# Kernel tuning notes

Hardware: AMD Instinct MI355X
Metric: run time of the kernel (lower is better)

## Reference

```python
import jax, jax.numpy as jnp
import numpy as np

NUM_HEADS = 8
DIM = 192  # target_dim = min(channels_list)
CHANNELS = [192, 384, 768]
SIZES = [(32, 32), (16, 16), (8, 8)]
BATCH = 4


def conv1x1(x, w, b):
    # x: [B,C,H,W], w: [O,C,1,1], b: [O]
    y = jnp.einsum('bchw,oc->bohw', x, w[:, :, 0, 0])
    return y + b[None, :, None, None]


def cross_attention(x, ctx, wq, wkv, wp, bp):
    # x: [B,N,C] queries, ctx: [B,M,C] key/value source
    B, N, C = x.shape
    M = ctx.shape[1]
    h = NUM_HEADS
    d = C // h
    scale = d ** -0.5
    q = (x @ wq.T).reshape(B, N, h, d).transpose(0, 2, 1, 3)          # [B,h,N,d]
    kv = ctx @ wkv.T                                                   # [B,M,2C]
    k = kv[..., :C].reshape(B, M, h, d).transpose(0, 2, 1, 3)          # [B,h,M,d]
    v = kv[..., C:].reshape(B, M, h, d).transpose(0, 2, 1, 3)          # [B,h,M,d]
    attn = jax.nn.softmax(jnp.einsum('bhnd,bhmd->bhnm', q, k) * scale, axis=-1)
    o = jnp.einsum('bhnm,bhmd->bhnd', attn, v)
    o = o.transpose(0, 2, 1, 3).reshape(B, N, C)
    return o @ wp.T + bp


def setup_inputs() -> dict:
    key = jax.random.key(0)
    ks = iter(jax.random.split(key, 64))
    s = 0.02
    inp = {}
    for i, (c, (H, W)) in enumerate(zip(CHANNELS, SIZES)):
        inp[f'f{i}'] = jax.random.normal(next(ks), (BATCH, c, H, W), dtype=jnp.float32)
    # input projections (scale 0 has c == target_dim -> Identity, no params)
    for i in (1, 2):
        c = CHANNELS[i]
        inp[f'proj{i}_w'] = jax.random.normal(next(ks), (DIM, c, 1, 1), dtype=jnp.float32) * s
        inp[f'proj{i}_b'] = jnp.zeros((DIM,), dtype=jnp.float32)
    # cross-attention params per scale (qkv_bias=False; proj has bias)
    for i in range(3):
        inp[f'q{i}_w'] = jax.random.normal(next(ks), (DIM, DIM), dtype=jnp.float32) * s
        inp[f'kv{i}_w'] = jax.random.normal(next(ks), (2 * DIM, DIM), dtype=jnp.float32) * s
        inp[f'pr{i}_w'] = jax.random.normal(next(ks), (DIM, DIM), dtype=jnp.float32) * s
        inp[f'pr{i}_b'] = jnp.zeros((DIM,), dtype=jnp.float32)
    # output projections back to each channel count
    for i, c in enumerate(CHANNELS):
        inp[f'out{i}_w'] = jax.random.normal(next(ks), (c, DIM, 1, 1), dtype=jnp.float32) * s
        inp[f'out{i}_b'] = jnp.zeros((c,), dtype=jnp.float32)
    return inp


def _forward(f0, f1, f2,
             proj1_w, proj1_b, proj2_w, proj2_b,
             q0_w, kv0_w, pr0_w, pr0_b,
             q1_w, kv1_w, pr1_w, pr1_b,
             q2_w, kv2_w, pr2_w, pr2_b,
             out0_w, out0_b, out1_w, out1_b, out2_w, out2_b):
    projected = [
        f0,  # Identity (channels == target_dim)
        conv1x1(f1, proj1_w, proj1_b),
        conv1x1(f2, proj2_w, proj2_b),
    ]
    attn_params = [
        (q0_w, kv0_w, pr0_w, pr0_b),
        (q1_w, kv1_w, pr1_w, pr1_b),
        (q2_w, kv2_w, pr2_w, pr2_b),
    ]
    out_params = [(out0_w, out0_b), (out1_w, out1_b), (out2_w, out2_b)]
    outputs = []
    for i in range(3):
        feat = projected[i]
        B, C, H, W = feat.shape
        x = feat.reshape(B, C, H * W).transpose(0, 2, 1)  # [B,N,C]
        ctxs = []
        for j in range(3):
            if j != i:
                r = jax.image.resize(projected[j], (B, C, H, W), method='bilinear', antialias=False)
                ctxs.append(r.reshape(B, C, H * W).transpose(0, 2, 1))
        ctx = jnp.concatenate(ctxs, axis=1)  # [B,M,C]
        enh = cross_attention(x, ctx, *attn_params[i])
        enh = enh.transpose(0, 2, 1).reshape(B, C, H, W) + feat
        outputs.append(conv1x1(enh, *out_params[i]))
    return tuple(outputs)


def reference(f0, f1, f2,
              proj1_w, proj1_b, proj2_w, proj2_b,
              q0_w, kv0_w, pr0_w, pr0_b,
              q1_w, kv1_w, pr1_w, pr1_b,
              q2_w, kv2_w, pr2_w, pr2_b,
              out0_w, out0_b, out1_w, out1_b, out2_w, out2_b):
    return _forward(f0, f1, f2,
                    proj1_w, proj1_b, proj2_w, proj2_b,
                    q0_w, kv0_w, pr0_w, pr0_b,
                    q1_w, kv1_w, pr1_w, pr1_b,
                    q2_w, kv2_w, pr2_w, pr2_b,
                    out0_w, out0_b, out1_w, out1_b, out2_w, out2_b)
```

## Files before the change

kernel.cpp:

```cpp
#include <hip/hip_runtime.h>
#include <math.h>

#define BB 4
#define DIM 192
#define HEADS 8
#define HD 24

typedef __attribute__((ext_vector_type(8))) short short8v;
typedef __attribute__((ext_vector_type(4))) short short4v;
typedef __attribute__((ext_vector_type(4))) float f32x4;
typedef __attribute__((ext_vector_type(4))) unsigned uint4v;

__device__ __forceinline__ short f2bf(float f) {
  unsigned u = __builtin_bit_cast(unsigned, f);
  u += 0x7FFF + ((u >> 16) & 1);
  return (short)(u >> 16);
}
__device__ __forceinline__ unsigned pk2(float a, float b) {
  unsigned r;
  asm("v_cvt_pk_bf16_f32 %0, %1, %2" : "=v"(r) : "v"(a), "v"(b));
  return r;
}
__device__ __forceinline__ float bf2f(unsigned u16) {
  return __builtin_bit_cast(float, u16 << 16);
}
__device__ __forceinline__ void gl_lds16(const void* g, void* l) {
  __builtin_amdgcn_global_load_lds(
      (const __attribute__((address_space(1))) unsigned int*)g,
      (__attribute__((address_space(3))) unsigned int*)l, 16, 0, 0);
}
__device__ __forceinline__ int xcd_swz(int bid, int nwg) {
  int q = nwg >> 3, r = nwg & 7;
  int xcd = bid & 7, idx = bid >> 3;
  return (xcd < r) ? (xcd * (q + 1) + idx) : (r * (q + 1) + (xcd - r) * q + idx);
}

struct PJob {
  int type;
  const float* s0; const float* s1; const float* s2;
  void* dst;
  int P0, P1v;
  int t_begin, t_end;
};
struct PJobs { PJob j[20]; };

__global__ __launch_bounds__(256) void prep_k(PJobs jobs, int nj) {
  int tid = blockIdx.x * 256 + threadIdx.x;
  for (int ji = 0; ji < 20; ++ji) {
    if (ji >= nj) return;
    PJob g = jobs.j[ji];
    if (tid < g.t_begin || tid >= g.t_end) continue;
    int t = tid - g.t_begin;
    if (g.type == 0) {
      float4 v = *(const float4*)&g.s0[(size_t)t * 4];
      uint2 u = {pk2(v.x, v.y), pk2(v.z, v.w)};
      *(uint2*)&((short*)g.dst)[(size_t)t * 4] = u;
    } else if (g.type == 1) {
      int X = g.P0, C = g.P1v, C8 = C >> 3;
      int x = t % X, c8 = (t / X) % C8, b = t / (X * C8);
      const float* s = g.s0 + ((size_t)b * C + c8 * 8) * X + x;
      float v[8];
#pragma unroll
      for (int j = 0; j < 8; ++j) v[j] = s[(size_t)j * X];
      uint4 u = {pk2(v[0], v[1]), pk2(v[2], v[3]), pk2(v[4], v[5]), pk2(v[6], v[7])};
      *(uint4*)&((short*)g.dst)[((size_t)b * X + x) * C + c8 * 8] = u;
    } else {
      int o = t;
      const float* w = g.s0 + (size_t)o * 192;
      float acc = g.s2[o];
      for (int k = 0; k < 192; ++k) acc += w[k] * g.s1[k];
      ((float*)g.dst)[o] = acc;
    }
    return;
  }
}

struct MJob {
  const short* A; const short* W; const float* bias; const float* T;
  void* out;
  int K, nOT, mode, tokPerB;
  float scale;
  int blk_begin, blk_end;
};
struct MJobs { MJob j[10]; };

__global__ __launch_bounds__(256) void mgemm_k(MJobs jobs, int nj, int nwg) {
  __shared__ short Asl[64 * 192];
  __shared__ short Wsl[64 * 192];
  int blk = xcd_swz(blockIdx.x, nwg);
  for (int ji = 0; ji < 10; ++ji) {
    if (ji >= nj) return;
    MJob g = jobs.j[ji];
    if (blk < g.blk_begin || blk >= g.blk_end) continue;
    int lb = blk - g.blk_begin;
    int ot = lb % g.nOT, tt = lb / g.nOT;
    int t0 = tt * 64, o0 = ot * 64;
    int tid = threadIdx.x, wv = tid >> 6, lane = tid & 63, c = lane & 15, qi = lane >> 4;
    const int K = g.K;
    int rowK[6];
#pragma unroll
    for (int i = 0; i < 6; ++i) {
      int o16 = i * 256 + tid;
      int row = o16 / 24, ch = o16 - row * 24;
      rowK[i] = row * K + ((ch ^ (row & 7)) << 3);
    }
    const short* Ab = g.A + (size_t)t0 * K;
    const short* Wb = g.W + (size_t)o0 * K;
    f32x4 acc[4];
#pragma unroll
    for (int jj = 0; jj < 4; ++jj) acc[jj] = (f32x4){0.f, 0.f, 0.f, 0.f};
    int nkc = K / 192;
    int swz = c & 7;
    for (int kc = 0; kc < nkc; ++kc) {
      if (kc) __syncthreads();
      int kco = kc * 192;
#pragma unroll
      for (int i = 0; i < 6; ++i) gl_lds16(Ab + rowK[i] + kco, &Asl[(i * 256 + wv * 64) * 8]);
#pragma unroll
      for (int i = 0; i < 6; ++i) gl_lds16(Wb + rowK[i] + kco, &Wsl[(i * 256 + wv * 64) * 8]);
      asm volatile("s_waitcnt vmcnt(0)" ::: "memory");
      __syncthreads();
      const short* Lb = (g.mode == 0) ? Wsl : Asl;
      const short* Rb = (g.mode == 0) ? Asl : Wsl;
      int lrow = wv * 16 + c;
#pragma unroll
      for (int ks = 0; ks < 6; ++ks) {
        int chx = ((ks * 4 + qi) ^ swz) << 3;
        short8v lf = *(const short8v*)&Lb[lrow * 192 + chx];
#pragma unroll
        for (int jj = 0; jj < 4; ++jj) {
          short8v rf = *(const short8v*)&Rb[(jj * 16 + c) * 192 + chx];
          acc[jj] = __builtin_amdgcn_mfma_f32_16x16x32_bf16(lf, rf, acc[jj], 0, 0, 0);
        }
      }
    }
    int OST = g.nOT * 64;
    if (g.mode == 0) {
      int ob = o0 + wv * 16 + (qi << 2);
      float4 bv = {0.f, 0.f, 0.f, 0.f};
      if (g.bias) bv = *(const float4*)&g.bias[ob];
      float s = g.scale;
      short* op = (short*)g.out;
#pragma unroll
      for (int jj = 0; jj < 4; ++jj) {
        size_t tok = t0 + jj * 16 + c;
        uint2 u = {pk2(acc[jj][0] * s + bv.x, acc[jj][1] * s + bv.y),
                   pk2(acc[jj][2] * s + bv.z, acc[jj][3] * s + bv.w)};
        *(uint2*)&op[tok * OST + ob] = u;
      }
    } else {
      int tokb = t0 + wv * 16;
      int b = tokb / g.tokPerB;
      int nl = tokb - b * g.tokPerB + (qi << 2);
#pragma unroll
      for (int jj = 0; jj < 4; ++jj) {
        int o = o0 + jj * 16 + c;
        if (g.mode == 1) {
          int np = (nl & ~31) + 8 * ((nl >> 2) & 3) + 4 * ((nl >> 4) & 1);
          size_t idx = ((size_t)b * OST + o) * g.tokPerB + np;
          uint2 u = {pk2(acc[jj][0], acc[jj][1]), pk2(acc[jj][2], acc[jj][3])};
          *(uint2*)&((short*)g.out)[idx] = u;
        } else if (g.mode == 2) {
          size_t idx = ((size_t)b * OST + o) * g.tokPerB + nl;
          float4 tv = *(const float4*)&g.T[idx];
          float4 ov = {acc[jj][0] + tv.x, acc[jj][1] + tv.y, acc[jj][2] + tv.z, acc[jj][3] + tv.w};
          *(float4*)&((float*)g.out)[idx] = ov;
        } else {
          size_t idx = ((size_t)b * OST + o) * g.tokPerB + nl;
          float bvv = g.bias ? g.bias[o] : 0.f;
          float4 ov = {acc[jj][0] + bvv, acc[jj][1] + bvv, acc[jj][2] + bvv, acc[jj][3] + bvv};
          *(float4*)&((float*)g.out)[idx] = ov;
        }
      }
    }
    return;
  }
}

struct RJob {
  const short* src;
  short* dst;
  int Hs, Ws, Wd, Mtot;
  float ry, rx;
  int t_begin, t_end;
};
struct RJobs { RJob j[6]; };

__global__ __launch_bounds__(256) void resize_k(RJobs jobs) {
  int tid = blockIdx.x * 256 + threadIdx.x;
  for (int ji = 0; ji < 6; ++ji) {
    RJob g = jobs.j[ji];
    if (tid < g.t_begin || tid >= g.t_end) continue;
    int t = tid - g.t_begin;
    int c8 = t % 24;
    int rest = t / 24;
    int HWd = g.Wd * g.Wd;
    int n = rest % HWd, b = rest / HWd;
    int y = n / g.Wd, x = n % g.Wd;
    float fy = (y + 0.5f) * g.ry - 0.5f;
    float fx = (x + 0.5f) * g.rx - 0.5f;
    int y0 = (int)floorf(fy), x0 = (int)floorf(fx);
    float wy = fy - (float)y0, wx = fx - (float)x0;
    int Hs = g.Hs, Ws = g.Ws;
    int y0c = min(max(y0, 0), Hs - 1), y1c = min(max(y0 + 1, 0), Hs - 1);
    int x0c = min(max(x0, 0), Ws - 1), x1c = min(max(x0 + 1, 0), Ws - 1);
    size_t sb = (size_t)b * Hs * Ws;
    const short* sp = g.src;
    uint4 u00 = *(const uint4*)&sp[(sb + y0c * Ws + x0c) * 192 + c8 * 8];
    uint4 u01 = *(const uint4*)&sp[(sb + y0c * Ws + x1c) * 192 + c8 * 8];
    uint4 u10 = *(const uint4*)&sp[(sb + y1c * Ws + x0c) * 192 + c8 * 8];
    uint4 u11 = *(const uint4*)&sp[(sb + y1c * Ws + x1c) * 192 + c8 * 8];
    float w00 = (1.f - wy) * (1.f - wx), w01 = (1.f - wy) * wx;
    float w10 = wy * (1.f - wx), w11 = wy * wx;
    unsigned a[4], bq[4], cq[4], dq[4];
    a[0]=u00.x; a[1]=u00.y; a[2]=u00.z; a[3]=u00.w;
    bq[0]=u01.x; bq[1]=u01.y; bq[2]=u01.z; bq[3]=u01.w;
    cq[0]=u10.x; cq[1]=u10.y; cq[2]=u10.z; cq[3]=u10.w;
    dq[0]=u11.x; dq[1]=u11.y; dq[2]=u11.z; dq[3]=u11.w;
    unsigned r[4];
#pragma unroll
    for (int k = 0; k < 4; ++k) {
      float lo = w00 * bf2f(a[k] & 0xffff) + w01 * bf2f(bq[k] & 0xffff) +
                 w10 * bf2f(cq[k] & 0xffff) + w11 * bf2f(dq[k] & 0xffff);
      float hi = w00 * bf2f(a[k] >> 16) + w01 * bf2f(bq[k] >> 16) +
                 w10 * bf2f(cq[k] >> 16) + w11 * bf2f(dq[k] >> 16);
      r[k] = pk2(lo, hi);
    }
    uint4 u = {r[0], r[1], r[2], r[3]};
    *(uint4*)&g.dst[((size_t)b * g.Mtot + n) * 192 + c8 * 8] = u;
    return;
  }
}

struct AJob {
  const short* q;
  const short* K;
  const short* V;
  short* o;
  int N, M;
  int blk_begin, blk_end;
};
struct AJobs { AJob j[3]; };

#define ABUF 7432
#define VBASE 3080

__global__ __launch_bounds__(256, 3) void attn_k(AJobs jobs, int cpx) {
  __shared__ __align__(16) short LDSbuf[3][ABUF];
  int bid = blockIdx.x;
  int blk = (bid & 7) * cpx + (bid >> 3);
  int tidx = threadIdx.x;
  if (tidx < 64) {
#pragma unroll
    for (int bb = 0; bb < 3; ++bb)
      ((int*)&LDSbuf[bb][VBASE + 24 * 136])[tidx] = 0x3F803F80;
  } else if (tidx < 76) {
    int bb = (tidx - 64) >> 2, e = (tidx - 64) & 3;
    ((int*)&LDSbuf[bb][3072])[e] = 0;
  }
  for (int ji = 0; ji < 3; ++ji) {
    AJob g = jobs.j[ji];
    if (blk < g.blk_begin || blk >= g.blk_end) continue;
    int lb = blk - g.blk_begin;
    const int N = g.N, M = g.M;
    int nch = N >> 6;
    int bh = lb / nch, ct = lb % nch;
    int b = bh >> 3, h = bh & 7;
    int wv = tidx >> 6, lane = tidx & 63;
    int c = lane & 15, qi = lane >> 4;
    int nw0 = (ct << 6) + (wv << 4);

    const short* Kg = g.K + (size_t)b * M * 192 + h * 24;
    const short* Vg = g.V + ((size_t)b * 192 + h * 24) * M;

    const short* gp[4];
    int gstr[4], loff[4];
    bool val[4];
#pragma unroll
    for (int i = 0; i < 4; ++i) {
      int s = tidx + (i << 8);
      val[i] = (s < 792);
      if (s < 384) {
        int row = s / 3, part = s - row * 3;
        gp[i] = Kg + row * 192 + part * 8;
        gstr[i] = 128 * 192;
        loff[i] = s * 8;
      } else {
        int v = s - 384;
        int row = v / 17, col = v - row * 17;
        int colc = (col < 16) ? col : 0;
        gp[i] = val[i] ? (Vg + (size_t)row * M + colc * 8) : Vg;
        gstr[i] = 128;
        loff[i] = VBASE + v * 8;
      }
    }

    short8v qf = *(const short8v*)&g.q[((size_t)b * N + nw0 + c) * 192 + h * 24 + (qi << 3)];
    if (qi == 3) {
#pragma unroll
      for (int j = 0; j < 8; ++j) qf[j] = 0;
    }

    f32x4 of0 = {0.f, 0.f, 0.f, 0.f}, of1 = {0.f, 0.f, 0.f, 0.f};
    const f32x4 zf = {0.f, 0.f, 0.f, 0.f};

    int nt = M >> 7;
#pragma unroll
    for (int i = 0; i < 4; ++i)
      if (val[i]) { gl_lds16(gp[i], &LDSbuf[0][loff[i]]); gp[i] += gstr[i]; }
    if (nt > 1) {
#pragma unroll
      for (int i = 0; i < 4; ++i)
        if (val[i]) { gl_lds16(gp[i], &LDSbuf[1][loff[i]]); gp[i] += gstr[i]; }
    }

    for (int t = 0; t < nt; ++t) {
      if (t + 1 < nt) asm volatile("s_waitcnt vmcnt(3) lgkmcnt(0)" ::: "memory");
      else            asm volatile("s_waitcnt vmcnt(0) lgkmcnt(0)" ::: "memory");
      __builtin_amdgcn_s_barrier();
      if (t + 2 < nt) {
        short* dst = LDSbuf[(t + 2) % 3];
#pragma unroll
        for (int i = 0; i < 4; ++i)
          if (val[i]) { gl_lds16(gp[i], &dst[loff[i]]); gp[i] += gstr[i]; }
      }
      const short* Kl = LDSbuf[t % 3];
      const short* Vl = Kl + VBASE;
      __builtin_amdgcn_s_setprio(1);
      f32x4 sr[8];
#pragma unroll
      for (int jj = 0; jj < 8; ++jj) {
        short8v kb = *(const short8v*)&Kl[(c + 16 * jj) * 24 + (qi << 3)];
        sr[jj] = __builtin_amdgcn_mfma_f32_16x16x32_bf16(kb, qf, zf, 0, 0, 0);
      }
      __builtin_amdgcn_s_setprio(0);
      unsigned pk[8][2];
#pragma unroll
      for (int jj = 0; jj < 8; ++jj) {
        float e0 = __builtin_amdgcn_exp2f(sr[jj][0]);
        float e1 = __builtin_amdgcn_exp2f(sr[jj][1]);
        float e2 = __builtin_amdgcn_exp2f(sr[jj][2]);
        float e3 = __builtin_amdgcn_exp2f(sr[jj][3]);
        pk[jj][0] = pk2(e0, e1);
        pk[jj][1] = pk2(e2, e3);
      }
      __builtin_amdgcn_s_setprio(1);
#pragma unroll
      for (int ks = 0; ks < 4; ++ks) {
        uint4v pu = {pk[2 * ks][0], pk[2 * ks][1], pk[2 * ks + 1][0], pk[2 * ks + 1][1]};
        short8v pa = __builtin_bit_cast(short8v, pu);
        short8v v0 = *(const short8v*)&Vl[c * 136 + ks * 32 + (qi << 3)];
        short8v v1 = *(const short8v*)&Vl[(16 + c) * 136 + ks * 32 + (qi << 3)];
        of0 = __builtin_amdgcn_mfma_f32_16x16x32_bf16(pa, v0, of0, 0, 0, 0);
        of1 = __builtin_amdgcn_mfma_f32_16x16x32_bf16(pa, v1, of1, 0, 0, 0);
      }
      __builtin_amdgcn_s_setprio(0);
    }
    float ls[4];
#pragma unroll
    for (int r = 0; r < 4; ++r) ls[r] = __shfl(of1[r], (qi << 4) + 8);
#pragma unroll
    for (int r = 0; r < 4; ++r) {
      float inv = 1.f / ls[r];
      int n = nw0 + (qi << 2) + r;
      short* op = g.o + ((size_t)b * N + n) * 192 + h * 24;
      op[c] = f2bf(of0[r] * inv);
      if (c < 8) op[16 + c] = f2bf(of1[r] * inv);
    }
    return;
  }
}

extern "C" void kernel_launch(void* const* d_in, const int* in_sizes, int n_in,
                              void* d_out, int out_size, void* d_ws, size_t ws_size,
                              hipStream_t stream) {
  (void)in_sizes; (void)n_in; (void)out_size; (void)ws_size;
  const float* f0 = (const float*)d_in[0];
  const float* f1 = (const float*)d_in[1];
  const float* f2 = (const float*)d_in[2];
  const float* p1w = (const float*)d_in[3];
  const float* p1b = (const float*)d_in[4];
  const float* p2w = (const float*)d_in[5];
  const float* p2b = (const float*)d_in[6];
  const float* qw[3]  = {(const float*)d_in[7],  (const float*)d_in[11], (const float*)d_in[15]};
  const float* kvw[3] = {(const float*)d_in[8],  (const float*)d_in[12], (const float*)d_in[16]};
  const float* prw[3] = {(const float*)d_in[9],  (const float*)d_in[13], (const float*)d_in[17]};
  const float* prb[3] = {(const float*)d_in[10], (const float*)d_in[14], (const float*)d_in[18]};
  const float* ow[3]  = {(const float*)d_in[19], (const float*)d_in[21], (const float*)d_in[23]};
  const float* ob[3]  = {(const float*)d_in[20], (const float*)d_in[22], (const float*)d_in[24]};

  char* ws = (char*)d_ws;
  short* x0    = (short*)(ws + 0);
  short* x1in  = (short*)(ws + 1572864);
  short* x2in  = (short*)(ws + 2359296);
  short* P1    = (short*)(ws + 2752512);
  short* P2    = (short*)(ws + 3145728);
  short* ctx0  = (short*)(ws + 3244032);
  short* ctx1  = (short*)(ws + 6389760);
  short* ctx2  = (short*)(ws + 7176192);
  short* qb    = (short*)(ws + 7372800);
  short* Kb    = (short*)(ws + 9437184);
  short* Vb    = (short*)(ws + 13565952);
  short* attb  = (short*)(ws + 17694720);
  float* T0    = (float*)(ws + 19759104);
  float* T1    = (float*)(ws + 22904832);
  float* T2    = (float*)(ws + 24477696);
  short* W2b   = (short*)(ws + 25264128);
  short* wcvt  = (short*)(ws + 25780224);
  float* bfin  = (float*)(ws + 27402240);
  short* prwT  = (short*)(ws + 27407616);

  short* p1w_b = wcvt;
  short* p2w_b = wcvt + 73728;
  short* qw_b[3]  = {wcvt + 221184, wcvt + 258048, wcvt + 294912};
  short* kvw_b[3] = {wcvt + 331776, wcvt + 405504, wcvt + 479232};
  short* ow_b[3]  = {wcvt + 552960, wcvt + 589824, wcvt + 663552};
  short* prwT_b[3] = {prwT, prwT + 36864, prwT + 73728};
  short* W2_b[3]  = {W2b, W2b + 36864, W2b + 110592};
  short* qs[3]  = {qb, qb + 786432, qb + 983040};
  short* Ks[3]  = {Kb, Kb + 1572864, Kb + 1966080};
  short* Vs[3]  = {Vb, Vb + 1572864, Vb + 1966080};
  short* atts[3] = {attb, attb + 786432, attb + 983040};
  float* out0 = (float*)d_out;
  float* outp[3] = {out0, out0 + 786432, out0 + 1179648};

  const int Ns[3] = {1024, 256, 64};
  const int Ms[3] = {2048, 512, 128};
  const int Couts[3] = {192, 384, 768};
  const float qsc = 0.2944888902728332f;

  {
    PJobs js{};
    int t0 = 0, n = 0;
    auto add = [&](PJob j, int tc) { j.t_begin = t0; j.t_end = t0 + tc; js.j[n++] = j; t0 += tc; };
    add({0, p1w, nullptr, nullptr, p1w_b, 0, 0, 0, 0}, 18432);
    add({0, p2w, nullptr, nullptr, p2w_b, 0, 0, 0, 0}, 36864);
    for (int i = 0; i < 3; ++i) add({0, qw[i], nullptr, nullptr, qw_b[i], 0, 0, 0, 0}, 9216);
    for (int i = 0; i < 3; ++i) add({0, kvw[i], nullptr, nullptr, kvw_b[i], 0, 0, 0, 0}, 18432);
    add({0, ow[0], nullptr, nullptr, ow_b[0], 0, 0, 0, 0}, 9216);
    add({0, ow[1], nullptr, nullptr, ow_b[1], 0, 0, 0, 0}, 18432);
    add({0, ow[2], nullptr, nullptr, ow_b[2], 0, 0, 0, 0}, 36864);
    add({1, f0, nullptr, nullptr, x0, 1024, 192, 0, 0}, 98304);
    add({1, f1, nullptr, nullptr, x1in, 256, 384, 0, 0}, 49152);
    add({1, f2, nullptr, nullptr, x2in, 64, 768, 0, 0}, 24576);
    for (int i = 0; i < 3; ++i)
      add({1, prw[i], nullptr, nullptr, prwT_b[i], 192, 192, 0, 0}, 4608);
    add({2, ow[0], prb[0], ob[0], bfin, 0, 0, 0, 0}, 192);
    add({2, ow[1], prb[1], ob[1], bfin + 192, 0, 0, 0, 0}, 384);
    add({2, ow[2], prb[2], ob[2], bfin + 576, 0, 0, 0, 0}, 768);
    hipLaunchKernelGGL(prep_k, dim3((t0 + 255) / 256), dim3(256), 0, stream, js, n);
  }
  {
    MJobs js{};
    int b0 = 0, n = 0;
    auto add = [&](MJob j, int nb) { j.blk_begin = b0; j.blk_end = b0 + nb; js.j[n++] = j; b0 += nb; };
    add({x1in, p1w_b, p1b, nullptr, P1, 384, 3, 0, 0, 1.f, 0, 0}, 16 * 3);
    add({x2in, p2w_b, p2b, nullptr, P2, 768, 3, 0, 0, 1.f, 0, 0}, 4 * 3);
    add({x0, qw_b[0], nullptr, nullptr, qs[0], 192, 3, 0, 0, qsc, 0, 0}, 64 * 3);
    add({x0, ow_b[0], bfin, nullptr, T0, 192, 3, 3, 1024, 1.f, 0, 0}, 64 * 3);
    for (int i = 0; i < 3; ++i)
      add({ow_b[i], prwT_b[i], nullptr, nullptr, W2_b[i], 192, 3, 0, 0, 1.f, 0, 0},
          (Couts[i] / 64) * 3);
    hipLaunchKernelGGL(mgemm_k, dim3(b0), dim3(256), 0, stream, js, n, b0);
  }
  {
    RJobs js{};
    int t0 = 0, n = 0;
    auto add = [&](RJob j, int tc) { j.t_begin = t0; j.t_end = t0 + tc; js.j[n++] = j; t0 += tc; };
    add({P1, ctx0, 16, 16, 32, 2048, 0.5f, 0.5f, 0, 0}, 98304);
    add({P2, ctx0 + 1024 * 192, 8, 8, 32, 2048, 0.25f, 0.25f, 0, 0}, 98304);
    add({x0, ctx1, 32, 32, 16, 512, 2.f, 2.f, 0, 0}, 24576);
    add({P2, ctx1 + 256 * 192, 8, 8, 16, 512, 0.5f, 0.5f, 0, 0}, 24576);
    add({x0, ctx2, 32, 32, 8, 128, 4.f, 4.f, 0, 0}, 6144);
    add({P1, ctx2 + 64 * 192, 16, 16, 8, 128, 2.f, 2.f, 0, 0}, 6144);
    hipLaunchKernelGGL(resize_k, dim3(t0 / 256), dim3(256), 0, stream, js);
  }
  {
    MJobs js{};
    int b0 = 0, n = 0;
    auto add = [&](MJob j, int nb) { j.blk_begin = b0; j.blk_end = b0 + nb; js.j[n++] = j; b0 += nb; };
    add({P1, qw_b[1], nullptr, nullptr, qs[1], 192, 3, 0, 0, qsc, 0, 0}, 16 * 3);
    add({P2, qw_b[2], nullptr, nullptr, qs[2], 192, 3, 0, 0, qsc, 0, 0}, 4 * 3);
    add({ctx0, kvw_b[0], nullptr, nullptr, Ks[0], 192, 3, 0, 0, 1.f, 0, 0}, 128 * 3);
    add({ctx1, kvw_b[1], nullptr, nullptr, Ks[1], 192, 3, 0, 0, 1.f, 0, 0}, 32 * 3);
    add({ctx2, kvw_b[2], nullptr, nullptr, Ks[2], 192, 3, 0, 0, 1.f, 0, 0}, 8 * 3);
    add({ctx0, kvw_b[0] + 36864, nullptr, nullptr, Vs[0], 192, 3, 1, 2048, 1.f, 0, 0}, 128 * 3);
    add({ctx1, kvw_b[1] + 36864, nullptr, nullptr, Vs[1], 192, 3, 1, 512, 1.f, 0, 0}, 32 * 3);
    add({ctx2, kvw_b[2] + 36864, nullptr, nullptr, Vs[2], 192, 3, 1, 128, 1.f, 0, 0}, 8 * 3);
    add({P1, ow_b[1], bfin + 192, nullptr, T1, 192, 6, 3, 256, 1.f, 0, 0}, 16 * 6);
    add({P2, ow_b[2], bfin + 576, nullptr, T2, 192, 12, 3, 64, 1.f, 0, 0}, 4 * 12);
    hipLaunchKernelGGL(mgemm_k, dim3(b0), dim3(256), 0, stream, js, n, b0);
  }
  {
    AJobs js{};
    int b0 = 0;
    for (int i = 0; i < 3; ++i) {
      int nb = BB * HEADS * (Ns[i] / 64);
      js.j[i] = {qs[i], Ks[i], Vs[i], atts[i], Ns[i], Ms[i], b0, b0 + nb};
      b0 += nb;
    }
    hipLaunchKernelGGL(attn_k, dim3(b0), dim3(256), 0, stream, js, b0 / 8);
  }
  {
    MJobs js{};
    int b0 = 0, n = 0;
    auto add = [&](MJob j, int nb) { j.blk_begin = b0; j.blk_end = b0 + nb; js.j[n++] = j; b0 += nb; };
    add({atts[0], W2_b[0], nullptr, T0, outp[0], 192, 3, 2, 1024, 1.f, 0, 0}, 64 * 3);
    add({atts[1], W2_b[1], nullptr, T1, outp[1], 192, 6, 2, 256, 1.f, 0, 0}, 16 * 6);
    add({atts[2], W2_b[2], nullptr, T2, outp[2], 192, 12, 2, 64, 1.f, 0, 0}, 4 * 12);
    hipLaunchKernelGGL(mgemm_k, dim3(b0), dim3(256), 0, stream, js, n, b0);
  }
}
```

Baseline: 75.97 us.

## Split KV tile across wave pairs with two query tiles per wave and LDS reduction

```diff
diff --git a/kernel.cpp b/kernel.cpp
--- a/kernel.cpp
+++ b/kernel.cpp
@@ -247,6 +247,7 @@
 
 __global__ __launch_bounds__(256, 3) void attn_k(AJobs jobs, int cpx) {
   __shared__ __align__(16) short LDSbuf[3][ABUF];
+  __shared__ __align__(16) float scr[2048];
   int bid = blockIdx.x;
   int blk = (bid & 7) * cpx + (bid >> 3);
   int tidx = threadIdx.x;
@@ -268,7 +269,8 @@
     int b = bh >> 3, h = bh & 7;
     int wv = tidx >> 6, lane = tidx & 63;
     int c = lane & 15, qi = lane >> 4;
-    int nw0 = (ct << 6) + (wv << 4);
+    int w1 = wv & 1, mh = wv >> 1;
+    int qbase = (ct << 6) + (w1 << 5);
 
     const short* Kg = g.K + (size_t)b * M * 192 + h * 24;
     const short* Vg = g.V + ((size_t)b * 192 + h * 24) * M;
@@ -295,13 +297,15 @@
       }
     }
 
-    short8v qf = *(const short8v*)&g.q[((size_t)b * N + nw0 + c) * 192 + h * 24 + (qi << 3)];
+    short8v qf1 = *(const short8v*)&g.q[((size_t)b * N + qbase + c) * 192 + h * 24 + (qi << 3)];
+    short8v qf2 = *(const short8v*)&g.q[((size_t)b * N + qbase + 16 + c) * 192 + h * 24 + (qi << 3)];
     if (qi == 3) {
 #pragma unroll
-      for (int j = 0; j < 8; ++j) qf[j] = 0;
+      for (int j = 0; j < 8; ++j) { qf1[j] = 0; qf2[j] = 0; }
     }
 
     f32x4 of0 = {0.f, 0.f, 0.f, 0.f}, of1 = {0.f, 0.f, 0.f, 0.f};
+    f32x4 of2 = {0.f, 0.f, 0.f, 0.f}, of3 = {0.f, 0.f, 0.f, 0.f};
     const f32x4 zf = {0.f, 0.f, 0.f, 0.f};
 
     int nt = M >> 7;
@@ -327,45 +331,74 @@
       const short* Kl = LDSbuf[t % 3];
       const short* Vl = Kl + VBASE;
       __builtin_amdgcn_s_setprio(1);
-      f32x4 sr[8];
-#pragma unroll
-      for (int jj = 0; jj < 8; ++jj) {
-        short8v kb = *(const short8v*)&Kl[(c + 16 * jj) * 24 + (qi << 3)];
-        sr[jj] = __builtin_amdgcn_mfma_f32_16x16x32_bf16(kb, qf, zf, 0, 0, 0);
+      f32x4 s1[4], s2[4];
+#pragma unroll
+      for (int jj = 0; jj < 4; ++jj) {
+        short8v kb = *(const short8v*)&Kl[((mh << 6) + c + 16 * jj) * 24 + (qi << 3)];
+        s1[jj] = __builtin_amdgcn_mfma_f32_16x16x32_bf16(kb, qf1, zf, 0, 0, 0);
+        s2[jj] = __builtin_amdgcn_mfma_f32_16x16x32_bf16(kb, qf2, zf, 0, 0, 0);
       }
       __builtin_amdgcn_s_setprio(0);
-      unsigned pk[8][2];
-#pragma unroll
-      for (int jj = 0; jj < 8; ++jj) {
-        float e0 = __builtin_amdgcn_exp2f(sr[jj][0]);
-        float e1 = __builtin_amdgcn_exp2f(sr[jj][1]);
-        float e2 = __builtin_amdgcn_exp2f(sr[jj][2]);
-        float e3 = __builtin_amdgcn_exp2f(sr[jj][3]);
-        pk[jj][0] = pk2(e0, e1);
-        pk[jj][1] = pk2(e2, e3);
+      unsigned pk1[4][2], pk2a[4][2];
+#pragma unroll
+      for (int jj = 0; jj < 4; ++jj) {
+        pk1[jj][0] = pk2(__builtin_amdgcn_exp2f(s1[jj][0]), __builtin_amdgcn_exp2f(s1[jj][1]));
+        pk1[jj][1] = pk2(__builtin_amdgcn_exp2f(s1[jj][2]), __builtin_amdgcn_exp2f(s1[jj][3]));
+        pk2a[jj][0] = pk2(__builtin_amdgcn_exp2f(s2[jj][0]), __builtin_amdgcn_exp2f(s2[jj][1]));
+        pk2a[jj][1] = pk2(__builtin_amdgcn_exp2f(s2[jj][2]), __builtin_amdgcn_exp2f(s2[jj][3]));
       }
       __builtin_amdgcn_s_setprio(1);
 #pragma unroll
-      for (int ks = 0; ks < 4; ++ks) {
-        uint4v pu = {pk[2 * ks][0], pk[2 * ks][1], pk[2 * ks + 1][0], pk[2 * ks + 1][1]};
-        short8v pa = __builtin_bit_cast(short8v, pu);
-        short8v v0 = *(const short8v*)&Vl[c * 136 + ks * 32 + (qi << 3)];
-        short8v v1 = *(const short8v*)&Vl[(16 + c) * 136 + ks * 32 + (qi << 3)];
-        of0 = __builtin_amdgcn_mfma_f32_16x16x32_bf16(pa, v0, of0, 0, 0, 0);
-        of1 = __builtin_amdgcn_mfma_f32_16x16x32_bf16(pa, v1, of1, 0, 0, 0);
+      for (int ks = 0; ks < 2; ++ks) {
+        uint4v pu1 = {pk1[2 * ks][0], pk1[2 * ks][1], pk1[2 * ks + 1][0], pk1[2 * ks + 1][1]};
+        uint4v pu2 = {pk2a[2 * ks][0], pk2a[2 * ks][1], pk2a[2 * ks + 1][0], pk2a[2 * ks + 1][1]};
+        short8v pa1 = __builtin_bit_cast(short8v, pu1);
+        short8v pa2 = __builtin_bit_cast(short8v, pu2);
+        int gcol = ((mh << 1) + ks) * 32 + (qi << 3);
+        short8v v0 = *(const short8v*)&Vl[c * 136 + gcol];
+        short8v v1 = *(const short8v*)&Vl[(16 + c) * 136 + gcol];
+        of0 = __builtin_amdgcn_mfma_f32_16x16x32_bf16(pa1, v0, of0, 0, 0, 0);
+        of1 = __builtin_amdgcn_mfma_f32_16x16x32_bf16(pa1, v1, of1, 0, 0, 0);
+        of2 = __builtin_amdgcn_mfma_f32_16x16x32_bf16(pa2, v0, of2, 0, 0, 0);
+        of3 = __builtin_amdgcn_mfma_f32_16x16x32_bf16(pa2, v1, of3, 0, 0, 0);
       }
       __builtin_amdgcn_s_setprio(0);
     }
-    float ls[4];
-#pragma unroll
-    for (int r = 0; r < 4; ++r) ls[r] = __shfl(of1[r], (qi << 4) + 8);
-#pragma unroll
-    for (int r = 0; r < 4; ++r) {
-      float inv = 1.f / ls[r];
-      int n = nw0 + (qi << 2) + r;
-      short* op = g.o + ((size_t)b * N + n) * 192 + h * 24;
-      op[c] = f2bf(of0[r] * inv);
-      if (c < 8) op[16 + c] = f2bf(of1[r] * inv);
+    if (mh) {
+      float* sp = &scr[w1 * 1024];
+      *(f32x4*)&sp[0 * 256 + lane * 4] = of0;
+      *(f32x4*)&sp[1 * 256 + lane * 4] = of1;
+      *(f32x4*)&sp[2 * 256 + lane * 4] = of2;
+      *(f32x4*)&sp[3 * 256 + lane * 4] = of3;
+    }
+    asm volatile("s_waitcnt lgkmcnt(0)" ::: "memory");
+    __builtin_amdgcn_sched_barrier(0);
+    __builtin_amdgcn_s_barrier();
+    if (!mh) {
+      const float* sp = &scr[w1 * 1024];
+      of0 += *(const f32x4*)&sp[0 * 256 + lane * 4];
+      of1 += *(const f32x4*)&sp[1 * 256 + lane * 4];
+      of2 += *(const f32x4*)&sp[2 * 256 + lane * 4];
+      of3 += *(const f32x4*)&sp[3 * 256 + lane * 4];
+      float ls1[4], ls2[4];
+#pragma unroll
+      for (int r = 0; r < 4; ++r) {
+        ls1[r] = __shfl(of1[r], (qi << 4) + 8);
+        ls2[r] = __shfl(of3[r], (qi << 4) + 8);
+      }
+#pragma unroll
+      for (int r = 0; r < 4; ++r) {
+        float inv1 = 1.f / ls1[r];
+        int n1 = qbase + (qi << 2) + r;
+        short* op1 = g.o + ((size_t)b * N + n1) * 192 + h * 24;
+        op1[c] = f2bf(of0[r] * inv1);
+        if (c < 8) op1[16 + c] = f2bf(of1[r] * inv1);
+        float inv2 = 1.f / ls2[r];
+        int n2 = qbase + 16 + (qi << 2) + r;
+        short* op2 = g.o + ((size_t)b * N + n2) * 192 + h * 24;
+        op2[c] = f2bf(of2[r] * inv2);
+        if (c < 8) op2[16 + c] = f2bf(of3[r] * inv2);
+      }
     }
     return;
   }
```

Result: no change. 74.75 us, median of 2 (-1.6%).
